# Performance work log

Hardware: AMD Instinct MI355X
Metric: run time of the kernel (lower is better)

## Reference

```python
import jax, jax.numpy as jnp
import numpy as np

EMBED = 512
HID = 16
BATCH = 4
SEQ = 1024


def setup_inputs() -> dict:
    key = jax.random.key(0)
    ks = jax.random.split(key, 8)
    e, h = EMBED, HID
    inputs = jax.random.normal(ks[0], (BATCH, SEQ, e), dtype=jnp.float32)
    # nn.Linear default init ~ U(-1/sqrt(fan_in), 1/sqrt(fan_in)); approximate scale
    Wq = jax.random.normal(ks[1], (e, e), dtype=jnp.float32) / np.sqrt(e)
    Wk = jax.random.normal(ks[2], (e, e), dtype=jnp.float32) / np.sqrt(e)
    Wv = jax.random.normal(ks[3], (e, e), dtype=jnp.float32) / np.sqrt(e)
    W1 = jax.random.normal(ks[4], (h, 2 * e), dtype=jnp.float32) / np.sqrt(2 * e)
    b1 = jnp.zeros((h,), dtype=jnp.float32)
    w2 = jax.random.normal(ks[5], (h,), dtype=jnp.float32) / np.sqrt(h)
    b2 = jnp.zeros((1,), dtype=jnp.float32)
    return {"inputs": inputs, "Wq": Wq, "Wk": Wk, "Wv": Wv,
            "W1": W1, "b1": b1, "w2": w2, "b2": b2}


def reference(inputs, Wq, Wk, Wv, W1, b1, w2, b2):
    e = inputs.shape[-1]
    # projections (torch Linear: x @ W.T)
    q = jnp.einsum('bse,fe->bsf', inputs, Wq)
    k = jnp.einsum('bse,fe->bsf', inputs, Wk)
    v = jnp.einsum('bse,fe->bsf', inputs, Wv)
    # attn_net Linear over concat [q_i; k_j] factorizes:
    # W1 @ [q;k] = W1[:, :e] @ q_i + W1[:, e:] @ k_j
    A = jnp.einsum('bse,he->bsh', q, W1[:, :e]) + b1  # (b, s, h)
    B = jnp.einsum('bse,he->bsh', k, W1[:, e:])       # (b, s, h)
    hidden = jnp.tanh(A[:, :, None, :] + B[:, None, :, :])  # (b, s, s, h)
    logits = jnp.einsum('bijh,h->bij', hidden, w2) + b2[0]   # (b, s, s)
    attn = jax.nn.softmax(logits, axis=-1)
    return jnp.einsum('bij,bjd->bid', attn, v)
```

## Files before the change

### kernel.cpp

```cpp
#include <hip/hip_runtime.h>
#include <math.h>
#include <stdint.h>

#define EMBED 512
#define HID 16
#define SEQ 1024

typedef unsigned short u16;
typedef __attribute__((ext_vector_type(8))) __bf16 bf16x8;
typedef __attribute__((ext_vector_type(4))) float f32x4;

__device__ __forceinline__ u16 f2bf(float f) {
    unsigned u = __float_as_uint(f);
    unsigned r = (u + 0x7FFFu + ((u >> 16) & 1u)) >> 16;
    return (u16)r;
}
__device__ __forceinline__ float bf2f(u16 h) {
    return __uint_as_float(((unsigned)h) << 16);
}
__device__ __forceinline__ void gload16(const void* g, void* d) {
    __builtin_amdgcn_global_load_lds(
        reinterpret_cast<const __attribute__((address_space(1))) unsigned int*>(
            reinterpret_cast<uintptr_t>(g)),
        reinterpret_cast<__attribute__((address_space(3))) unsigned int*>(
            reinterpret_cast<uintptr_t>(d)),
        16, 0, 0);
}

__global__ __launch_bounds__(256) void prep_kernel(
    const float* __restrict__ Wq, const float* __restrict__ Wk,
    const float* __restrict__ W1, const float* __restrict__ Wvm,
    const float* __restrict__ x,
    u16* __restrict__ AH, u16* __restrict__ AL, u16* __restrict__ x_hi)
{
    __shared__ float w1s[EMBED];
    int t = threadIdx.x;
    int blk = blockIdx.x;
    if (blk < 64) {
        int h2 = blk >> 1, half = blk & 1;
        int ab = h2 >> 4, h = h2 & 15;
        const float* Wmat = ab ? Wk : Wq;
        const float* w1row = W1 + (size_t)h * (2 * EMBED) + ab * EMBED;
        for (int f = t; f < EMBED; f += 256) w1s[f] = w1row[f];
        __syncthreads();
        int e0 = (half << 8) + t;
        float acc = 0.f;
        #pragma unroll 16
        for (int f = 0; f < EMBED; ++f)
            acc += w1s[f] * Wmat[(size_t)f * EMBED + e0];
        u16 hi = f2bf(acc);
        AH[(size_t)(512 + h2) * EMBED + e0] = hi;
        AL[(size_t)(512 + h2) * EMBED + e0] = f2bf(acc - bf2f(hi));
        AH[(size_t)(544 + h2) * EMBED + e0] = 0;
        AL[(size_t)(544 + h2) * EMBED + e0] = 0;
    } else if (blk < 320) {
        int i = (blk - 64) * 256 + t;
        float4 v = ((const float4*)Wvm)[i];
        u16 h0 = f2bf(v.x), h1 = f2bf(v.y), h2 = f2bf(v.z), h3 = f2bf(v.w);
        ((ushort4*)AH)[i] = make_ushort4(h0, h1, h2, h3);
        ((ushort4*)AL)[i] = make_ushort4(f2bf(v.x - bf2f(h0)), f2bf(v.y - bf2f(h1)),
                                         f2bf(v.z - bf2f(h2)), f2bf(v.w - bf2f(h3)));
    } else {
        int i = (blk - 320) * 256 + t;
        float4 v = ((const float4*)x)[i];
        ((ushort4*)x_hi)[i] = make_ushort4(f2bf(v.x), f2bf(v.y), f2bf(v.z), f2bf(v.w));
    }
}

template<int NR>
__device__ __forceinline__ void stageR(const u16* src, int ld, int kt,
                                       u16* ldsb, int t)
{
    int kb0 = kt << 7;
    #pragma unroll
    for (int i = 0; i < NR / 32; ++i) {
        int row  = i * 32 + (t >> 3);
        int colb = (((t & 7) ^ ((t >> 3) & 7)) << 4);
        const char* g = (const char*)src + (size_t)row * ((size_t)ld * 2) + kb0 + colb;
        gload16(g, (char*)ldsb + i * 4096 + ((t >> 6) << 10) + ((t & 63) << 4));
    }
}
__device__ __forceinline__ bf16x8 ldfrag(const u16* ldsb, int r, int s) {
    return *(const bf16x8*)((const char*)ldsb + r * 128 + (((s ^ (r & 7))) << 4));
}

__global__ __launch_bounds__(256, 3) void gemm_kernel(
    const u16* __restrict__ AH, const u16* __restrict__ AL,
    const u16* __restrict__ Bh, const float* __restrict__ b1,
    u16* __restrict__ VT, float* __restrict__ EAt, float* __restrict__ EBt)
{
    const float K2 = 2.8853900817779268f;
    __shared__ __attribute__((aligned(16))) u16 lds[24576];
    int t = threadIdx.x;
    int l = t & 63, wid = t >> 6;
    int wm = (wid >> 1) * 32, wn = (wid & 1) * 32;
    int lin = blockIdx.y * 64 + blockIdx.x;
    int v = (lin & 7) * 72 + (lin >> 3);
    int mt = v % 9, nt = v / 9;
    int m0 = mt * 64, n0 = nt * 64;
    const u16* pAh = AH + (size_t)m0 * EMBED;
    const u16* pAl = AL + (size_t)m0 * EMBED;
    const u16* pBh = Bh + (size_t)n0 * EMBED;
    f32x4 acc[2][2] = {};
    const bool two = (mt == 8);

    for (int kp = 0; kp < 4; ++kp) {
        stageR<64>(pAh, EMBED, 2 * kp,     lds,         t);
        if (two) stageR<64>(pAl, EMBED, 2 * kp,     lds + 4096,  t);
        stageR<64>(pBh, EMBED, 2 * kp,     lds + 8192,  t);
        stageR<64>(pAh, EMBED, 2 * kp + 1, lds + 12288, t);
        if (two) stageR<64>(pAl, EMBED, 2 * kp + 1, lds + 16384, t);
        stageR<64>(pBh, EMBED, 2 * kp + 1, lds + 20480, t);
        __syncthreads();
        #pragma unroll
        for (int half = 0; half < 2; ++half) {
            u16* lAh = lds + half * 12288;
            u16* lAl = lAh + 4096;
            u16* lB  = lAh + 8192;
            #pragma unroll
            for (int kk = 0; kk < 2; ++kk) {
                int sb = (kk << 2) + (l >> 4);
                bf16x8 ah[2], bh[2];
                #pragma unroll
                for (int mf = 0; mf < 2; ++mf)
                    ah[mf] = ldfrag(lAh, wm + mf * 16 + (l & 15), sb);
                #pragma unroll
                for (int nf = 0; nf < 2; ++nf)
                    bh[nf] = ldfrag(lB, wn + nf * 16 + (l & 15), sb);
                if (two) {
                    bf16x8 al2[2];
                    #pragma unroll
                    for (int mf = 0; mf < 2; ++mf)
                        al2[mf] = ldfrag(lAl, wm + mf * 16 + (l & 15), sb);
                    #pragma unroll
                    for (int mf = 0; mf < 2; ++mf)
                        #pragma unroll
                        for (int nf = 0; nf < 2; ++nf) {
                            acc[mf][nf] = __builtin_amdgcn_mfma_f32_16x16x32_bf16(ah[mf],  bh[nf], acc[mf][nf], 0, 0, 0);
                            acc[mf][nf] = __builtin_amdgcn_mfma_f32_16x16x32_bf16(al2[mf], bh[nf], acc[mf][nf], 0, 0, 0);
                        }
                } else {
                    #pragma unroll
                    for (int mf = 0; mf < 2; ++mf)
                        #pragma unroll
                        for (int nf = 0; nf < 2; ++nf)
                            acc[mf][nf] = __builtin_amdgcn_mfma_f32_16x16x32_bf16(ah[mf], bh[nf], acc[mf][nf], 0, 0, 0);
                }
            }
        }
        __syncthreads();
    }

    int cr = (l >> 4) << 2, cc = l & 15;
    #pragma unroll
    for (int mf = 0; mf < 2; ++mf)
        #pragma unroll
        for (int nf = 0; nf < 2; ++nf)
            #pragma unroll
            for (int r = 0; r < 4; ++r) {
                int gr = m0 + wm + mf * 16 + cr + r;
                int col = n0 + wn + nf * 16 + cc;
                float v2 = acc[mf][nf][r];
                if (gr < 512) {
                    VT[(size_t)gr * 4096 + col] = f2bf(v2);
                } else if (gr < 528) {
                    EAt[(size_t)(gr - 512) * 4096 + col] =
                        __builtin_amdgcn_exp2f(K2 * (v2 + b1[gr - 512]));
                } else if (gr < 544) {
                    EBt[(size_t)(gr - 528) * 4096 + col] =
                        __builtin_amdgcn_exp2f(K2 * v2);
                }
            }
}

__global__ __launch_bounds__(256) void attn_kernel(
    const float* __restrict__ EAt, const float* __restrict__ EBt,
    const float* __restrict__ w2, u16* __restrict__ P)
{
    const float L2E = 1.4426950408889634f;
    __shared__ float redA[4], redB[4];
    int blk = blockIdx.x;
    int b = blk >> 9;
    int i0 = (blk & 511) << 1;
    int t = threadIdx.x;
    int gA = (b << 10) + i0;

    float ax[HID], ay[HID];
    #pragma unroll
    for (int h = 0; h < HID; ++h) {
        ax[h] = EAt[(size_t)h * 4096 + gA];
        ay[h] = EAt[(size_t)h * 4096 + gA + 1];
    }

    float P1a[8], P2a[8], PSa[8];
    #pragma unroll
    for (int p = 0; p < 8; ++p) {
        float w1 = -2.f * w2[2 * p], w2_ = -2.f * w2[2 * p + 1];
        P1a[p] = w1; P2a[p] = w2_; PSa[p] = w1 + w2_;
    }
    float S0 = 0.f;
    #pragma unroll
    for (int p = 0; p < 8; ++p) S0 += fmaxf(P1a[p], 0.f) + fmaxf(P2a[p], 0.f);

    const float* EBb = EBt + (b << 10);
    float pa0, pa1, pa2, pa3, pb0, pb1, pb2, pb3;

#define DOC(c, PA, PB) { \
    int j = t + (c) * 256; \
    float bb[HID]; \
    _Pragma("unroll") \
    for (int h = 0; h < HID; ++h) bb[h] = EBb[(size_t)h * 4096 + j]; \
    float sA = 0.f, sB = 0.f; \
    _Pragma("unroll") \
    for (int q = 0; q < 4; ++q) { \
        int h0 = q << 2, p0 = q << 1, p1 = p0 + 1; \
        { float e1 = ax[h0]*bb[h0], e2 = ax[h0+1]*bb[h0+1]; \
          float e3 = ax[h0+2]*bb[h0+2], e4 = ax[h0+3]*bb[h0+3]; \
          float D12 = fmaf(e1, e2, e1) + (e2 + 1.0f); \
          float N12 = fmaf(P2a[p0], e1, fmaf(P1a[p0], e2, PSa[p0])); \
          float D34 = fmaf(e3, e4, e3) + (e4 + 1.0f); \
          float N34 = fmaf(P2a[p1], e3, fmaf(P1a[p1], e4, PSa[p1])); \
          sA = fmaf(fmaf(N12, D34, N34 * D12), __builtin_amdgcn_rcpf(D12 * D34), sA); } \
        { float e1 = ay[h0]*bb[h0], e2 = ay[h0+1]*bb[h0+1]; \
          float e3 = ay[h0+2]*bb[h0+2], e4 = ay[h0+3]*bb[h0+3]; \
          float D12 = fmaf(e1, e2, e1) + (e2 + 1.0f); \
          float N12 = fmaf(P2a[p0], e1, fmaf(P1a[p0], e2, PSa[p0])); \
          float D34 = fmaf(e3, e4, e3) + (e4 + 1.0f); \
          float N34 = fmaf(P2a[p1], e3, fmaf(P1a[p1], e4, PSa[p1])); \
          sB = fmaf(fmaf(N12, D34, N34 * D12), __builtin_amdgcn_rcpf(D12 * D34), sB); } \
    } \
    PA = __builtin_amdgcn_exp2f((sA - S0) * L2E); \
    PB = __builtin_amdgcn_exp2f((sB - S0) * L2E); }

    DOC(0, pa0, pb0)
    DOC(1, pa1, pb1)
    DOC(2, pa2, pb2)
    DOC(3, pa3, pb3)
#undef DOC

    float sA = (pa0 + pa1) + (pa2 + pa3);
    float sB = (pb0 + pb1) + (pb2 + pb3);
    #pragma unroll
    for (int o = 32; o > 0; o >>= 1) {
        sA += __shfl_xor(sA, o);
        sB += __shfl_xor(sB, o);
    }
    if ((t & 63) == 0) { redA[t >> 6] = sA; redB[t >> 6] = sB; }
    __syncthreads();
    float invA = __fdividef(1.f, (redA[0] + redA[1]) + (redA[2] + redA[3]));
    float invB = __fdividef(1.f, (redB[0] + redB[1]) + (redB[2] + redB[3]));

    size_t baseA = ((size_t)(b * SEQ) + i0) * SEQ;
    size_t baseB = baseA + SEQ;
    P[baseA + t      ] = f2bf(pa0 * invA);
    P[baseA + t + 256] = f2bf(pa1 * invA);
    P[baseA + t + 512] = f2bf(pa2 * invA);
    P[baseA + t + 768] = f2bf(pa3 * invA);
    P[baseB + t      ] = f2bf(pb0 * invB);
    P[baseB + t + 256] = f2bf(pb1 * invB);
    P[baseB + t + 512] = f2bf(pb2 * invB);
    P[baseB + t + 768] = f2bf(pb3 * invB);
}

__global__ __launch_bounds__(256, 2) void pv_kernel(
    const u16* __restrict__ P, const u16* __restrict__ VT,
    float* __restrict__ out)
{
    __shared__ __attribute__((aligned(16))) u16 lds[32768];
    int t = threadIdx.x;
    int l = t & 63, wid = t >> 6;
    int wm = (wid >> 1) * 32, wn = (wid & 1) * 32;
    int lin = (blockIdx.z << 7) + (blockIdx.y << 3) + blockIdx.x;
    int v = (lin & 7) * 64 + (lin >> 3);
    int zb = v >> 7;
    int w_ = v & 127;
    int m0 = (w_ >> 3) * 64, n0 = (w_ & 7) * 64;
    const u16* pA = P + (size_t)zb * SEQ * SEQ + (size_t)m0 * SEQ;
    const u16* pB = VT + (size_t)n0 * 4096 + ((size_t)zb << 10);

    f32x4 acc[2][2] = {};

    auto STAGE = [&](int buf, int kp) {
        u16* base = lds + buf * 16384;
        stageR<64>(pA, SEQ,  2 * kp,     base,         t);
        stageR<64>(pB, 4096, 2 * kp,     base + 4096,  t);
        stageR<64>(pA, SEQ,  2 * kp + 1, base + 8192,  t);
        stageR<64>(pB, 4096, 2 * kp + 1, base + 12288, t);
    };
    auto COMPUTE = [&](int buf) {
        #pragma unroll
        for (int half = 0; half < 2; ++half) {
            u16* lA = lds + buf * 16384 + half * 8192;
            u16* lB = lA + 4096;
            #pragma unroll
            for (int kk = 0; kk < 2; ++kk) {
                int sb = (kk << 2) + (l >> 4);
                bf16x8 af[2], bf_[2];
                #pragma unroll
                for (int mf = 0; mf < 2; ++mf)
                    af[mf] = ldfrag(lA, wm + mf * 16 + (l & 15), sb);
                #pragma unroll
                for (int nf = 0; nf < 2; ++nf)
                    bf_[nf] = ldfrag(lB, wn + nf * 16 + (l & 15), sb);
                #pragma unroll
                for (int mf = 0; mf < 2; ++mf)
                    #pragma unroll
                    for (int nf = 0; nf < 2; ++nf)
                        acc[mf][nf] = __builtin_amdgcn_mfma_f32_16x16x32_bf16(af[mf], bf_[nf], acc[mf][nf], 0, 0, 0);
            }
        }
    };

    STAGE(0, 0);
    __syncthreads();
    int cur = 0;
    for (int kp = 0; kp + 1 < 8; ++kp) {
        STAGE(cur ^ 1, kp + 1);
        COMPUTE(cur);
        __syncthreads();
        cur ^= 1;
    }
    COMPUTE(cur);

    int cr = (l >> 4) << 2, cc = l & 15;
    #pragma unroll
    for (int mf = 0; mf < 2; ++mf)
        #pragma unroll
        for (int nf = 0; nf < 2; ++nf)
            #pragma unroll
            for (int r = 0; r < 4; ++r)
                out[((size_t)(zb * SEQ) + m0 + wm + mf * 16 + cr + r) * EMBED
                    + n0 + wn + nf * 16 + cc] = acc[mf][nf][r];
}

extern "C" void kernel_launch(void* const* d_in, const int* in_sizes, int n_in,
                              void* d_out, int out_size, void* d_ws, size_t ws_size,
                              hipStream_t stream) {
    const float* x   = (const float*)d_in[0];
    const float* Wq  = (const float*)d_in[1];
    const float* Wk  = (const float*)d_in[2];
    const float* Wvm = (const float*)d_in[3];
    const float* W1  = (const float*)d_in[4];
    const float* b1  = (const float*)d_in[5];
    const float* w2  = (const float*)d_in[6];

    char* ws = (char*)d_ws;
    u16*   AH   = (u16*)(ws + 0);
    u16*   AL   = (u16*)(ws + 589824);
    u16*   x_hi = (u16*)(ws + 1179648);
    u16*   VT   = (u16*)(ws + 5373952);
    float* EAt  = (float*)(ws + 9568256);
    float* EBt  = (float*)(ws + 9830400);
    u16*   P    = (u16*)(ws + 10092544);
    float* out  = (float*)d_out;

    hipLaunchKernelGGL(prep_kernel, dim3(2368), dim3(256), 0, stream,
                       Wq, Wk, W1, Wvm, x, AH, AL, x_hi);
    hipLaunchKernelGGL(gemm_kernel, dim3(64, 9), dim3(256), 0, stream,
                       AH, AL, x_hi, b1, VT, EAt, EBt);
    hipLaunchKernelGGL(attn_kernel, dim3(2048), dim3(256), 0, stream,
                       EAt, EBt, w2, P);
    hipLaunchKernelGGL(pv_kernel, dim3(8, 16, 4), dim3(256), 0, stream,
                       P, VT, out);
}
```

Before: 54.42 us.

## Process four query rows per attn block and split gemm into specialized paths

The attention kernel now handles four query rows per block instead of two, so each loaded EB column vector is reused across four rows and the grid is halved. This cuts global loads of EBt per output. The gemm kernel separates the two-operand (AH+AL) tile path from the common single-operand path; the latter stages four k-slices per barrier using a larger LDS buffer, which halves the number of sync rounds. The larger LDS footprint lowers the gemm occupancy target from 3 to 2 blocks, and the extra per-row registers in attn may reduce its occupancy.

```diff
diff --git a/kernel.cpp b/kernel.cpp
--- a/kernel.cpp
+++ b/kernel.cpp
@@ -84,13 +84,13 @@
     return *(const bf16x8*)((const char*)ldsb + r * 128 + (((s ^ (r & 7))) << 4));
 }
 
-__global__ __launch_bounds__(256, 3) void gemm_kernel(
+__global__ __launch_bounds__(256, 2) void gemm_kernel(
     const u16* __restrict__ AH, const u16* __restrict__ AL,
     const u16* __restrict__ Bh, const float* __restrict__ b1,
     u16* __restrict__ VT, float* __restrict__ EAt, float* __restrict__ EBt)
 {
     const float K2 = 2.8853900817779268f;
-    __shared__ __attribute__((aligned(16))) u16 lds[24576];
+    __shared__ __attribute__((aligned(16))) u16 lds[32768];
     int t = threadIdx.x;
     int l = t & 63, wid = t >> 6;
     int wm = (wid >> 1) * 32, wn = (wid & 1) * 32;
@@ -104,34 +104,32 @@
     f32x4 acc[2][2] = {};
     const bool two = (mt == 8);
 
-    for (int kp = 0; kp < 4; ++kp) {
-        stageR<64>(pAh, EMBED, 2 * kp,     lds,         t);
-        if (two) stageR<64>(pAl, EMBED, 2 * kp,     lds + 4096,  t);
-        stageR<64>(pBh, EMBED, 2 * kp,     lds + 8192,  t);
-        stageR<64>(pAh, EMBED, 2 * kp + 1, lds + 12288, t);
-        if (two) stageR<64>(pAl, EMBED, 2 * kp + 1, lds + 16384, t);
-        stageR<64>(pBh, EMBED, 2 * kp + 1, lds + 20480, t);
-        __syncthreads();
-        #pragma unroll
-        for (int half = 0; half < 2; ++half) {
-            u16* lAh = lds + half * 12288;
-            u16* lAl = lAh + 4096;
-            u16* lB  = lAh + 8192;
-            #pragma unroll
-            for (int kk = 0; kk < 2; ++kk) {
-                int sb = (kk << 2) + (l >> 4);
-                bf16x8 ah[2], bh[2];
+    if (two) {
+        for (int kp = 0; kp < 4; ++kp) {
+            stageR<64>(pAh, EMBED, 2 * kp,     lds,         t);
+            stageR<64>(pAl, EMBED, 2 * kp,     lds + 4096,  t);
+            stageR<64>(pBh, EMBED, 2 * kp,     lds + 8192,  t);
+            stageR<64>(pAh, EMBED, 2 * kp + 1, lds + 12288, t);
+            stageR<64>(pAl, EMBED, 2 * kp + 1, lds + 16384, t);
+            stageR<64>(pBh, EMBED, 2 * kp + 1, lds + 20480, t);
+            __syncthreads();
+            #pragma unroll
+            for (int half = 0; half < 2; ++half) {
+                u16* lAh = lds + half * 12288;
+                u16* lAl = lAh + 4096;
+                u16* lB  = lAh + 8192;
                 #pragma unroll
-                for (int mf = 0; mf < 2; ++mf)
-                    ah[mf] = ldfrag(lAh, wm + mf * 16 + (l & 15), sb);
-                #pragma unroll
-                for (int nf = 0; nf < 2; ++nf)
-                    bh[nf] = ldfrag(lB, wn + nf * 16 + (l & 15), sb);
-                if (two) {
-                    bf16x8 al2[2];
-                    #pragma unroll
-                    for (int mf = 0; mf < 2; ++mf)
+                for (int kk = 0; kk < 2; ++kk) {
+                    int sb = (kk << 2) + (l >> 4);
+                    bf16x8 ah[2], al2[2], bh[2];
+                    #pragma unroll
+                    for (int mf = 0; mf < 2; ++mf) {
+                        ah[mf]  = ldfrag(lAh, wm + mf * 16 + (l & 15), sb);
                         al2[mf] = ldfrag(lAl, wm + mf * 16 + (l & 15), sb);
+                    }
+                    #pragma unroll
+                    for (int nf = 0; nf < 2; ++nf)
+                        bh[nf] = ldfrag(lB, wn + nf * 16 + (l & 15), sb);
                     #pragma unroll
                     for (int mf = 0; mf < 2; ++mf)
                         #pragma unroll
@@ -139,7 +137,32 @@
                             acc[mf][nf] = __builtin_amdgcn_mfma_f32_16x16x32_bf16(ah[mf],  bh[nf], acc[mf][nf], 0, 0, 0);
                             acc[mf][nf] = __builtin_amdgcn_mfma_f32_16x16x32_bf16(al2[mf], bh[nf], acc[mf][nf], 0, 0, 0);
                         }
-                } else {
+                }
+            }
+            __syncthreads();
+        }
+    } else {
+        for (int kq = 0; kq < 2; ++kq) {
+            #pragma unroll
+            for (int q = 0; q < 4; ++q) {
+                stageR<64>(pAh, EMBED, 4 * kq + q, lds + q * 8192,        t);
+                stageR<64>(pBh, EMBED, 4 * kq + q, lds + q * 8192 + 4096, t);
+            }
+            __syncthreads();
+            #pragma unroll
+            for (int q = 0; q < 4; ++q) {
+                u16* lAh = lds + q * 8192;
+                u16* lB  = lAh + 4096;
+                #pragma unroll
+                for (int kk = 0; kk < 2; ++kk) {
+                    int sb = (kk << 2) + (l >> 4);
+                    bf16x8 ah[2], bh[2];
+                    #pragma unroll
+                    for (int mf = 0; mf < 2; ++mf)
+                        ah[mf] = ldfrag(lAh, wm + mf * 16 + (l & 15), sb);
+                    #pragma unroll
+                    for (int nf = 0; nf < 2; ++nf)
+                        bh[nf] = ldfrag(lB, wn + nf * 16 + (l & 15), sb);
                     #pragma unroll
                     for (int mf = 0; mf < 2; ++mf)
                         #pragma unroll
@@ -147,8 +170,8 @@
                             acc[mf][nf] = __builtin_amdgcn_mfma_f32_16x16x32_bf16(ah[mf], bh[nf], acc[mf][nf], 0, 0, 0);
                 }
             }
+            __syncthreads();
         }
-        __syncthreads();
     }
 
     int cr = (l >> 4) << 2, cc = l & 15;
@@ -178,18 +201,18 @@
     const float* __restrict__ w2, u16* __restrict__ P)
 {
     const float L2E = 1.4426950408889634f;
-    __shared__ float redA[4], redB[4];
+    __shared__ float redA[4], redB[4], redC[4], redD[4];
     int blk = blockIdx.x;
-    int b = blk >> 9;
-    int i0 = (blk & 511) << 1;
+    int b = blk >> 8;
+    int i0 = (blk & 255) << 2;
     int t = threadIdx.x;
     int gA = (b << 10) + i0;
 
-    float ax[HID], ay[HID];
+    float ax[HID], ay[HID], az[HID], aw[HID];
     #pragma unroll
     for (int h = 0; h < HID; ++h) {
-        ax[h] = EAt[(size_t)h * 4096 + gA];
-        ay[h] = EAt[(size_t)h * 4096 + gA + 1];
+        const float* Er = EAt + (size_t)h * 4096 + gA;
+        ax[h] = Er[0]; ay[h] = Er[1]; az[h] = Er[2]; aw[h] = Er[3];
     }
 
     float P1a[8], P2a[8], PSa[8];
@@ -204,54 +227,65 @@
 
     const float* EBb = EBt + (b << 10);
     float pa0, pa1, pa2, pa3, pb0, pb1, pb2, pb3;
-
-#define DOC(c, PA, PB) { \
+    float pc0, pc1, pc2, pc3, pd0, pd1, pd2, pd3;
+
+#define ROWSUM(S, AV) { \
+    _Pragma("unroll") \
+    for (int q = 0; q < 4; ++q) { \
+        int h0 = q << 2, p0 = q << 1, p1 = p0 + 1; \
+        float e1 = AV[h0]*bb[h0], e2 = AV[h0+1]*bb[h0+1]; \
+        float e3 = AV[h0+2]*bb[h0+2], e4 = AV[h0+3]*bb[h0+3]; \
+        float D12 = fmaf(e1, e2, e1) + (e2 + 1.0f); \
+        float N12 = fmaf(P2a[p0], e1, fmaf(P1a[p0], e2, PSa[p0])); \
+        float D34 = fmaf(e3, e4, e3) + (e4 + 1.0f); \
+        float N34 = fmaf(P2a[p1], e3, fmaf(P1a[p1], e4, PSa[p1])); \
+        S = fmaf(fmaf(N12, D34, N34 * D12), __builtin_amdgcn_rcpf(D12 * D34), S); \
+    } }
+
+#define DOC(c, PA, PB, PC, PD) { \
     int j = t + (c) * 256; \
     float bb[HID]; \
     _Pragma("unroll") \
     for (int h = 0; h < HID; ++h) bb[h] = EBb[(size_t)h * 4096 + j]; \
-    float sA = 0.f, sB = 0.f; \
-    _Pragma("unroll") \
-    for (int q = 0; q < 4; ++q) { \
-        int h0 = q << 2, p0 = q << 1, p1 = p0 + 1; \
-        { float e1 = ax[h0]*bb[h0], e2 = ax[h0+1]*bb[h0+1]; \
-          float e3 = ax[h0+2]*bb[h0+2], e4 = ax[h0+3]*bb[h0+3]; \
-          float D12 = fmaf(e1, e2, e1) + (e2 + 1.0f); \
-          float N12 = fmaf(P2a[p0], e1, fmaf(P1a[p0], e2, PSa[p0])); \
-          float D34 = fmaf(e3, e4, e3) + (e4 + 1.0f); \
-          float N34 = fmaf(P2a[p1], e3, fmaf(P1a[p1], e4, PSa[p1])); \
-          sA = fmaf(fmaf(N12, D34, N34 * D12), __builtin_amdgcn_rcpf(D12 * D34), sA); } \
-        { float e1 = ay[h0]*bb[h0], e2 = ay[h0+1]*bb[h0+1]; \
-          float e3 = ay[h0+2]*bb[h0+2], e4 = ay[h0+3]*bb[h0+3]; \
-          float D12 = fmaf(e1, e2, e1) + (e2 + 1.0f); \
-          float N12 = fmaf(P2a[p0], e1, fmaf(P1a[p0], e2, PSa[p0])); \
-          float D34 = fmaf(e3, e4, e3) + (e4 + 1.0f); \
-          float N34 = fmaf(P2a[p1], e3, fmaf(P1a[p1], e4, PSa[p1])); \
-          sB = fmaf(fmaf(N12, D34, N34 * D12), __builtin_amdgcn_rcpf(D12 * D34), sB); } \
-    } \
+    float sA = 0.f, sB = 0.f, sC = 0.f, sD = 0.f; \
+    ROWSUM(sA, ax) ROWSUM(sB, ay) ROWSUM(sC, az) ROWSUM(sD, aw) \
     PA = __builtin_amdgcn_exp2f((sA - S0) * L2E); \
-    PB = __builtin_amdgcn_exp2f((sB - S0) * L2E); }
-
-    DOC(0, pa0, pb0)
-    DOC(1, pa1, pb1)
-    DOC(2, pa2, pb2)
-    DOC(3, pa3, pb3)
+    PB = __builtin_amdgcn_exp2f((sB - S0) * L2E); \
+    PC = __builtin_amdgcn_exp2f((sC - S0) * L2E); \
+    PD = __builtin_amdgcn_exp2f((sD - S0) * L2E); }
+
+    DOC(0, pa0, pb0, pc0, pd0)
+    DOC(1, pa1, pb1, pc1, pd1)
+    DOC(2, pa2, pb2, pc2, pd2)
+    DOC(3, pa3, pb3, pc3, pd3)
 #undef DOC
+#undef ROWSUM
 
     float sA = (pa0 + pa1) + (pa2 + pa3);
     float sB = (pb0 + pb1) + (pb2 + pb3);
+    float sC = (pc0 + pc1) + (pc2 + pc3);
+    float sD = (pd0 + pd1) + (pd2 + pd3);
     #pragma unroll
     for (int o = 32; o > 0; o >>= 1) {
         sA += __shfl_xor(sA, o);
         sB += __shfl_xor(sB, o);
-    }
-    if ((t & 63) == 0) { redA[t >> 6] = sA; redB[t >> 6] = sB; }
+        sC += __shfl_xor(sC, o);
+        sD += __shfl_xor(sD, o);
+    }
+    if ((t & 63) == 0) {
+        redA[t >> 6] = sA; redB[t >> 6] = sB;
+        redC[t >> 6] = sC; redD[t >> 6] = sD;
+    }
     __syncthreads();
     float invA = __fdividef(1.f, (redA[0] + redA[1]) + (redA[2] + redA[3]));
     float invB = __fdividef(1.f, (redB[0] + redB[1]) + (redB[2] + redB[3]));
+    float invC = __fdividef(1.f, (redC[0] + redC[1]) + (redC[2] + redC[3]));
+    float invD = __fdividef(1.f, (redD[0] + redD[1]) + (redD[2] + redD[3]));
 
     size_t baseA = ((size_t)(b * SEQ) + i0) * SEQ;
     size_t baseB = baseA + SEQ;
+    size_t baseC = baseB + SEQ;
+    size_t baseD = baseC + SEQ;
     P[baseA + t      ] = f2bf(pa0 * invA);
     P[baseA + t + 256] = f2bf(pa1 * invA);
     P[baseA + t + 512] = f2bf(pa2 * invA);
@@ -260,6 +294,14 @@
     P[baseB + t + 256] = f2bf(pb1 * invB);
     P[baseB + t + 512] = f2bf(pb2 * invB);
     P[baseB + t + 768] = f2bf(pb3 * invB);
+    P[baseC + t      ] = f2bf(pc0 * invC);
+    P[baseC + t + 256] = f2bf(pc1 * invC);
+    P[baseC + t + 512] = f2bf(pc2 * invC);
+    P[baseC + t + 768] = f2bf(pc3 * invC);
+    P[baseD + t      ] = f2bf(pd0 * invD);
+    P[baseD + t + 256] = f2bf(pd1 * invD);
+    P[baseD + t + 512] = f2bf(pd2 * invD);
+    P[baseD + t + 768] = f2bf(pd3 * invD);
 }
 
 __global__ __launch_bounds__(256, 2) void pv_kernel(
@@ -358,7 +400,7 @@
                        Wq, Wk, W1, Wvm, x, AH, AL, x_hi);
     hipLaunchKernelGGL(gemm_kernel, dim3(64, 9), dim3(256), 0, stream,
                        AH, AL, x_hi, b1, VT, EAt, EBt);
-    hipLaunchKernelGGL(attn_kernel, dim3(2048), dim3(256), 0, stream,
+    hipLaunchKernelGGL(attn_kernel, dim3(1024), dim3(256), 0, stream,
                        EAt, EBt, w2, P);
     hipLaunchKernelGGL(pv_kernel, dim3(8, 16, 4), dim3(256), 0, stream,
                        P, VT, out);
```

Measured after the change: 55.41 us. About the same (+1.8%).
